# Kernel optimization log

Measured on AMD Instinct MI355X. Metric: run time of the kernel, lower is better.

Reference implementation:

```python
import jax, jax.numpy as jnp
import numpy as np

B, S, HID = 2, 1024, 2048
NH, NKV, HD = 16, 4, 128
SCALE = 1.0 / np.sqrt(HD)
ROPE_BASE = 10000.0
EPS = 1e-6


def setup_inputs() -> dict:
    key = jax.random.key(0)
    ks = jax.random.split(key, 5)
    std = 0.02
    return {
        "hidden_states": jax.random.normal(ks[0], (B, S, HID), jnp.float32),
        "Wq": jax.random.normal(ks[1], (NH * HD, HID), jnp.float32) * std,
        "Wk": jax.random.normal(ks[2], (NKV * HD, HID), jnp.float32) * std,
        "Wv": jax.random.normal(ks[3], (NKV * HD, HID), jnp.float32) * std,
        "Wo": jax.random.normal(ks[4], (HID, HID), jnp.float32) * std,
        "q_norm_w": jnp.ones((HD,), jnp.float32),
        "k_norm_w": jnp.ones((HD,), jnp.float32),
    }


def _rope(x):
    # x: [B, H, S, D]; half-split rotary
    d2 = HD // 2
    inv_freq = 1.0 / (ROPE_BASE ** (jnp.arange(0, HD, 2, dtype=jnp.float32) / HD))
    ang = jnp.arange(S, dtype=jnp.float32)[:, None] * inv_freq[None, :]  # [S, d2]
    cos, sin = jnp.cos(ang), jnp.sin(ang)
    x1, x2 = x[..., :d2], x[..., d2:]
    return jnp.concatenate([x1 * cos - x2 * sin, x1 * sin + x2 * cos], axis=-1)


def _rms(x, w):
    var = jnp.mean(jnp.square(x), axis=-1, keepdims=True)
    return x * jax.lax.rsqrt(var + EPS) * w


def reference(hidden_states, Wq, Wk, Wv, Wo, q_norm_w, k_norm_w):
    b, s, _ = hidden_states.shape
    # projections (no bias)
    q = (hidden_states @ Wq.T).reshape(b, s, NH, HD).transpose(0, 2, 1, 3)
    k = (hidden_states @ Wk.T).reshape(b, s, NKV, HD).transpose(0, 2, 1, 3)
    v = (hidden_states @ Wv.T).reshape(b, s, NKV, HD).transpose(0, 2, 1, 3)
    # RoPE then per-head-dim RMS qk-norm (shared params across heads)
    q, k = _rope(q), _rope(k)
    q, k = _rms(q, q_norm_w), _rms(k, k_norm_w)
    # GQA: repeat kv heads
    groups = NH // NKV
    k = jnp.repeat(k, groups, axis=1)
    v = jnp.repeat(v, groups, axis=1)
    # stick-breaking attention, strictly causal (attend_current=False), no normalize
    logits = jnp.einsum("bhid,bhjd->bhij", q, k) * SCALE  # [B,H,S,S]
    log_p = jax.nn.log_sigmoid(logits)
    log_om = jax.nn.log_sigmoid(-logits)  # log(1 - p)
    i = jnp.arange(s)
    mask = i[None, :] < i[:, None]  # j < i
    masked_om = jnp.where(mask, log_om, 0.0)
    # cum[i,j] = sum_{j < k < i} log(1-p[i,k]) : exclusive reversed cumsum
    cum = jnp.flip(jnp.cumsum(jnp.flip(masked_om, -1), -1), -1) - masked_om
    att = jnp.where(mask, jnp.exp(log_p + cum), 0.0)
    o = jnp.einsum("bhij,bhjd->bhid", att, v)
    o = o.transpose(0, 2, 1, 3).reshape(b, s, NH * HD)
    return o @ Wo.T
```

## Files before the change

kernel.cpp:

```cpp
#include <hip/hip_runtime.h>
#include <math.h>

#define B_    2
#define S_    1024
#define HID_  2048
#define NH_   16
#define NKV_  4
#define HD_   128
#define GROUPS (NH_ / NKV_)
#define SCALE_ 0.08838834764831845f

#define NZ_   2
#define QPSZ  4194304
#define KPSZ  1048576

typedef _Float16 f16x8 __attribute__((ext_vector_type(8)));
typedef _Float16 f16x4 __attribute__((ext_vector_type(4)));
typedef float    f32x4 __attribute__((ext_vector_type(4)));

__device__ __forceinline__ void async_copy16(const void* g, void* l) {
    __builtin_amdgcn_global_load_lds(
        (const __attribute__((address_space(1))) void*)g,
        (__attribute__((address_space(3))) void*)l, 16, 0, 0);
}

__device__ __forceinline__ int dpp_swap1(int x) {
    return __builtin_amdgcn_update_dpp(0, x, 0xB1, 0xF, 0xF, true);
}

__global__ __launch_bounds__(256) void cast5_f16(
    const float4* __restrict__ s0, ushort4* __restrict__ d0, int n0,
    const float4* __restrict__ s1, ushort4* __restrict__ d1, int n1,
    const float4* __restrict__ s2, ushort4* __restrict__ d2, int n2,
    const float4* __restrict__ s3, ushort4* __restrict__ d3, int n3,
    const float4* __restrict__ s4, ushort4* __restrict__ d4, int n4)
{
    int i = blockIdx.x * 256 + threadIdx.x;
    const float4* s; ushort4* d; int idx;
    if (i < n0)                          { s = s0; d = d0; idx = i; }
    else if (i < n0 + n1)                { s = s1; d = d1; idx = i - n0; }
    else if (i < n0 + n1 + n2)           { s = s2; d = d2; idx = i - n0 - n1; }
    else if (i < n0 + n1 + n2 + n3)      { s = s3; d = d3; idx = i - n0 - n1 - n2; }
    else if (i < n0 + n1 + n2 + n3 + n4) { s = s4; d = d4; idx = i - n0 - n1 - n2 - n3; }
    else return;
    float4 v = s[idx];
    _Float16 a = (_Float16)v.x, b = (_Float16)v.y,
             c = (_Float16)v.z, e = (_Float16)v.w;
    ushort4 o;
    o.x = *(unsigned short*)&a; o.y = *(unsigned short*)&b;
    o.z = *(unsigned short*)&c; o.w = *(unsigned short*)&e;
    d[idx] = o;
}

__global__ __launch_bounds__(256) void qkv_gemm(
    const _Float16* __restrict__ A,
    const _Float16* __restrict__ Wq,
    const _Float16* __restrict__ Wk,
    const _Float16* __restrict__ Wv,
    _Float16* __restrict__ Qp,
    _Float16* __restrict__ Kp,
    _Float16* __restrict__ Vp)
{
    __shared__ __align__(16) unsigned char smem[32768];

    const int tid  = threadIdx.x;
    const int lane = tid & 63, wave = tid >> 6;
    const int wr = (wave >> 1) * 64, wc = (wave & 1) * 64;
    const int bm = blockIdx.y * 128;
    const int bt = blockIdx.x;
    const int z  = blockIdx.z;
    const int kbase = z * (HID_ / NZ_);

    const _Float16* Wsel;
    _Float16* Csel;
    int nrow0, heads;
    if (bt < 16)      { Wsel = Wq; Csel = Qp + (size_t)z * QPSZ; nrow0 = bt * 128;        heads = NH_;  }
    else if (bt < 20) { Wsel = Wk; Csel = Kp + (size_t)z * KPSZ; nrow0 = (bt - 16) * 128; heads = NKV_; }
    else              { Wsel = Wv; Csel = Vp + (size_t)z * KPSZ; nrow0 = (bt - 20) * 128; heads = NKV_; }

    const int srow = 32 * wave + (lane >> 2);
    const int scol = (((lane & 3) ^ ((lane >> 3) & 3))) * 8;
    const _Float16* Ag = A    + (size_t)(bm + srow)    * HID_ + kbase + scol;
    const _Float16* Wg = Wsel + (size_t)(nrow0 + srow) * HID_ + kbase + scol;

    const unsigned aoff = (unsigned)(wave * 2048);

    f32x4 acc[4][4];
    const f32x4 fz = {0.f, 0.f, 0.f, 0.f};
#pragma unroll
    for (int i = 0; i < 4; i++)
#pragma unroll
        for (int j = 0; j < 4; j++) acc[i][j] = fz;

    const int ml = lane & 15, kg = lane >> 4;
    const int kgx = kg ^ ((ml >> 1) & 3);

#define QKV_STAGE(d, k0) do {                                                 \
        _Float16* la_ = (_Float16*)(smem + (d) * 16384 + aoff);               \
        _Float16* lw_ = (_Float16*)(smem + (d) * 16384 + 8192 + aoff);        \
        async_copy16(Ag + (k0), la_);                                         \
        async_copy16(Ag + (k0) + (size_t)16 * HID_, la_ + 16 * 32);           \
        async_copy16(Wg + (k0), lw_);                                         \
        async_copy16(Wg + (k0) + (size_t)16 * HID_, lw_ + 16 * 32);           \
    } while (0)

#define QKV_COMPUTE(d) do {                                                   \
        const _Float16* tA = (const _Float16*)(smem + (d) * 16384);           \
        const _Float16* tW = (const _Float16*)(smem + (d) * 16384 + 8192);    \
        f16x8 a[4], b[4];                                                     \
        _Pragma("unroll")                                                     \
        for (int mi = 0; mi < 4; mi++)                                        \
            a[mi] = *(const f16x8*)&tA[(wr + mi * 16 + ml) * 32 + kgx * 8];   \
        _Pragma("unroll")                                                     \
        for (int ni = 0; ni < 4; ni++)                                        \
            b[ni] = *(const f16x8*)&tW[(wc + ni * 16 + ml) * 32 + kgx * 8];   \
        _Pragma("unroll")                                                     \
        for (int mi = 0; mi < 4; mi++)                                        \
            _Pragma("unroll")                                                 \
            for (int ni = 0; ni < 4; ni++)                                    \
                acc[mi][ni] = __builtin_amdgcn_mfma_f32_16x16x32_f16(         \
                    a[mi], b[ni], acc[mi][ni], 0, 0, 0);                      \
    } while (0)

    QKV_STAGE(0, 0);
    asm volatile("s_waitcnt vmcnt(0)" ::: "memory");
    __builtin_amdgcn_s_barrier();

    int d = 0;
    for (int t = 0; t < 31; t++) {
        QKV_STAGE(d ^ 1, (t + 1) * 32);
        asm volatile("s_waitcnt vmcnt(4)" ::: "memory");
        __builtin_amdgcn_s_barrier();
        __builtin_amdgcn_sched_barrier(0);

        QKV_COMPUTE(d);

        __builtin_amdgcn_sched_barrier(0);
        __builtin_amdgcn_s_barrier();
        d ^= 1;
    }
    asm volatile("s_waitcnt vmcnt(0)" ::: "memory");
    __builtin_amdgcn_s_barrier();
    __builtin_amdgcn_sched_barrier(0);
    QKV_COMPUTE(d);
#undef QKV_STAGE
#undef QKV_COMPUTE

#pragma unroll
    for (int mi = 0; mi < 4; mi++) {
#pragma unroll
        for (int ni = 0; ni < 4; ni++) {
#pragma unroll
            for (int r = 0; r < 4; r++) {
                int m = bm + wr + mi * 16 + kg * 4 + r;
                int n = nrow0 + wc + ni * 16 + ml;
                int hh = n >> 7, d2 = n & 127;
                int b_ = m >> 10, s = m & 1023;
                size_t idx = (((size_t)(b_ * heads + hh)) * S_ + s) * HD_ + d2;
                Csel[idx] = (_Float16)acc[mi][ni][r];
            }
        }
    }
}

__global__ __launch_bounds__(512) void out_gemm(
    const _Float16* __restrict__ A,
    const _Float16* __restrict__ W,
    float* __restrict__ Cout)
{
    __shared__ __align__(16) unsigned char smem[66560];

    const int tid  = threadIdx.x;
    const int lane = tid & 63, wave = tid >> 6;
    const int kh = wave >> 2;
    const int wv = wave & 3;
    const int wr = (wv >> 1) * 64, wc = (wv & 1) * 64;
    const int bm = blockIdx.y * 128, bn = blockIdx.x * 128;
    const int kbase = kh * (HID_ / 2);

    const int srow = 32 * wv + (lane >> 2);
    const int scol = (((lane & 3) ^ ((lane >> 3) & 3))) * 8;
    const _Float16* Ag = A + (size_t)(bm + srow) * HID_ + kbase + scol;
    const _Float16* Wg = W + (size_t)(bn + srow) * HID_ + kbase + scol;

    const unsigned aoff = (unsigned)(kh * 8192 + 32 * wv * 64);
    const unsigned woff = (unsigned)(16384 + kh * 8192 + 32 * wv * 64);

    f32x4 acc[4][4];
    const f32x4 fz = {0.f, 0.f, 0.f, 0.f};
#pragma unroll
    for (int i = 0; i < 4; i++)
#pragma unroll
        for (int j = 0; j < 4; j++) acc[i][j] = fz;

    const int ml = lane & 15, kg = lane >> 4;
    const int kgx = kg ^ ((ml >> 1) & 3);

#define OG_STAGE(d, k0) do {                                                  \
        _Float16* la_ = (_Float16*)(smem + (d) * 32768 + aoff);               \
        _Float16* lw_ = (_Float16*)(smem + (d) * 32768 + woff);               \
        async_copy16(Ag + (k0), la_);                                         \
        async_copy16(Ag + (k0) + (size_t)16 * HID_, la_ + 16 * 32);           \
        async_copy16(Wg + (k0), lw_);                                         \
        async_copy16(Wg + (k0) + (size_t)16 * HID_, lw_ + 16 * 32);           \
    } while (0)

#define OG_COMPUTE(d) do {                                                    \
        const _Float16* tA = (const _Float16*)(smem + (d) * 32768 + kh * 8192);\
        const _Float16* tW = (const _Float16*)(smem + (d) * 32768 + 16384 + kh * 8192);\
        f16x8 a[4], b[4];                                                     \
        _Pragma("unroll")                                                     \
        for (int mi = 0; mi < 4; mi++)                                        \
            a[mi] = *(const f16x8*)&tA[(wr + mi * 16 + ml) * 32 + kgx * 8];   \
        _Pragma("unroll")                                                     \
        for (int ni = 0; ni < 4; ni++)                                        \
            b[ni] = *(const f16x8*)&tW[(wc + ni * 16 + ml) * 32 + kgx * 8];   \
        _Pragma("unroll")                                                     \
        for (int mi = 0; mi < 4; mi++)                                        \
            _Pragma("unroll")                                                 \
            for (int ni = 0; ni < 4; ni++)                                    \
                acc[mi][ni] = __builtin_amdgcn_mfma_f32_16x16x32_f16(         \
                    a[mi], b[ni], acc[mi][ni], 0, 0, 0);                      \
    } while (0)

    OG_STAGE(0, 0);
    asm volatile("s_waitcnt vmcnt(0)" ::: "memory");
    __builtin_amdgcn_s_barrier();

    int d = 0;
    for (int t = 0; t < 31; t++) {
        OG_STAGE(d ^ 1, (t + 1) * 32);
        asm volatile("s_waitcnt vmcnt(4)" ::: "memory");
        __builtin_amdgcn_s_barrier();
        __builtin_amdgcn_sched_barrier(0);

        OG_COMPUTE(d);

        __builtin_amdgcn_sched_barrier(0);
        __builtin_amdgcn_s_barrier();
        d ^= 1;
    }
    asm volatile("s_waitcnt vmcnt(0)" ::: "memory");
    __builtin_amdgcn_s_barrier();
    __builtin_amdgcn_sched_barrier(0);
    OG_COMPUTE(d);
#undef OG_STAGE
#undef OG_COMPUTE

    __syncthreads();
    float* red = (float*)smem;
    float* rp  = red + ((size_t)(wv * 64 + lane)) * 65;
    if (kh == 1) {
#pragma unroll
        for (int mi = 0; mi < 4; mi++)
#pragma unroll
            for (int ni = 0; ni < 4; ni++)
#pragma unroll
                for (int r = 0; r < 4; r++)
                    rp[mi * 16 + ni * 4 + r] = acc[mi][ni][r];
    }
    __syncthreads();
    if (kh == 0) {
#pragma unroll
        for (int mi = 0; mi < 4; mi++)
#pragma unroll
            for (int ni = 0; ni < 4; ni++)
#pragma unroll
                for (int r = 0; r < 4; r++) {
                    float v = acc[mi][ni][r] + rp[mi * 16 + ni * 4 + r];
                    int m = bm + wr + mi * 16 + kg * 4 + r;
                    int n = bn + wc + ni * 16 + ml;
                    Cout[(size_t)m * HID_ + n] = v;
                }
    }
}

__global__ __launch_bounds__(256) void rope_rms_v(
    const _Float16* __restrict__ Qp, const _Float16* __restrict__ Kp,
    const _Float16* __restrict__ Vp,
    const float* __restrict__ qw, const float* __restrict__ kw,
    _Float16* __restrict__ Qout, _Float16* __restrict__ Kout,
    _Float16* __restrict__ Vout)
{
    int row = blockIdx.x * 4 + (threadIdx.x >> 6);
    int lane = threadIdx.x & 63;

    if (row >= 40960) {
        int lrow = row - 40960;
        size_t off = (size_t)lrow * HD_ + lane * 2;
        float a0 = 0.f, a1 = 0.f;
#pragma unroll
        for (int zp = 0; zp < NZ_; zp++) {
            a0 += (float)Vp[(size_t)zp * KPSZ + off];
            a1 += (float)Vp[(size_t)zp * KPSZ + off + 1];
        }
        _Float16* q = Vout + (size_t)lrow * HD_;
        q[lane * 2]     = (_Float16)a0;
        q[lane * 2 + 1] = (_Float16)a1;
        return;
    }

    bool isQ = row < 32768;
    int lrow = isQ ? row : row - 32768;
    const _Float16* p0 = isQ ? Qp : Kp;
    size_t psz = isQ ? QPSZ : KPSZ;
    _Float16* q = (isQ ? Qout : Kout) + (size_t)lrow * HD_;
    const float* w = isQ ? qw : kw;
    int s = row & (S_ - 1);

    size_t base = (size_t)lrow * HD_;
    float x1 = 0.f, x2 = 0.f;
#pragma unroll
    for (int zp = 0; zp < NZ_; zp++) {
        x1 += (float)p0[(size_t)zp * psz + base + lane];
        x2 += (float)p0[(size_t)zp * psz + base + lane + 64];
    }

    float invf = __builtin_amdgcn_exp2f(-(float)lane * 0.2076205059304601f);
    float ang = (float)s * invf;
    float sn = __sinf(ang);
    float c  = __cosf(ang);

    float y1 = x1 * c - x2 * sn;
    float y2 = x1 * sn + x2 * c;

    float ss = y1 * y1 + y2 * y2;
#pragma unroll
    for (int off = 32; off > 0; off >>= 1) ss += __shfl_xor(ss, off);

    float scl = rsqrtf(ss * (1.0f / 128.0f) + 1e-6f);
    q[lane]      = (_Float16)(y1 * scl * w[lane]);
    q[lane + 64] = (_Float16)(y2 * scl * w[lane + 64]);
}

#define QK_STR 136
#define VT_STR 72
#define SS_STR 68
#define AT_STR 72

__global__ __launch_bounds__(512) void stick_attn(
    const _Float16* __restrict__ Q, const _Float16* __restrict__ K,
    const _Float16* __restrict__ V, _Float16* __restrict__ AO)
{
    __shared__ __align__(16) _Float16 Qs[64][QK_STR];
    __shared__ __align__(16) _Float16 Ks[64][QK_STR];
    __shared__ __align__(16) _Float16 Vt[128][VT_STR];
    __shared__ __align__(16) float    Ss[64][SS_STR];
    __shared__ __align__(16) _Float16 atts[64][AT_STR];
    __shared__ float paccs[64];

    const int bid = blockIdx.x;
    const int slot = bid & 255, phase = bid >> 8;
    const int hb = slot >> 3, iw = slot & 7;
    const int b = hb >> 4, h = hb & 15;
    const int qb = phase ? iw : 15 - iw;

    const int kvh = h / GROUPS;
    const int tid = threadIdx.x;
    const int lane = tid & 63, wave = tid >> 6;
    const int qw = wave >> 1;
    const int kh = wave & 1;
    const int ml = lane & 15, quad = lane >> 4;

    const _Float16* Kbase = K + ((size_t)(b * NKV_ + kvh) * S_) * HD_;
    const _Float16* Vbase = V + ((size_t)(b * NKV_ + kvh) * S_) * HD_;

    const f32x4 fz = {0.f, 0.f, 0.f, 0.f};

    const int qi0 = qb * 64;
    const _Float16* Qbase = Q + ((size_t)(b * NH_ + h) * S_ + qi0) * HD_;

    const int kr = tid >> 4, kc = (tid & 15) * 8;
    const _Float16* Vrow = Vbase + (size_t)lane * HD_ + wave * 16;

    f16x8 kA, kB, vA, vB;
    {
        const _Float16* kp = Kbase + (size_t)(qb * 64 + kr) * HD_ + kc;
        kA = *(const f16x8*)(kp);
        kB = *(const f16x8*)(kp + (size_t)32 * HD_);
        const _Float16* vp = Vrow + (size_t)(qb * 64) * HD_;
        vA = *(const f16x8*)(vp);
        vB = *(const f16x8*)(vp + 8);
    }

    for (int idx = tid; idx < 64 * 16; idx += 512) {
        int r = idx >> 4, c8 = (idx & 15) * 8;
        *(f16x8*)&Qs[r][c8] = *(const f16x8*)(Qbase + r * HD_ + c8);
    }
    if (tid < 64) paccs[tid] = 1.f;
    __syncthreads();

    f16x8 aq[4];
#pragma unroll
    for (int ks = 0; ks < 4; ks++)
        aq[ks] = *(const f16x8*)&Qs[qw * 16 + ml][ks * 32 + quad * 8];

    f32x4 accO[4] = {fz, fz, fz, fz};

    for (int kb = qb; kb >= 0; --kb) {
        __syncthreads();

        *(f16x8*)&Ks[kr][kc]      = kA;
        *(f16x8*)&Ks[kr + 32][kc] = kB;

        {
            int4 i0 = *(int4*)&vA, i1 = *(int4*)&vB;
            int4 p0, p1;
            p0.x = dpp_swap1(i0.x); p0.y = dpp_swap1(i0.y);
            p0.z = dpp_swap1(i0.z); p0.w = dpp_swap1(i0.w);
            p1.x = dpp_swap1(i1.x); p1.y = dpp_swap1(i1.y);
            p1.z = dpp_swap1(i1.z); p1.w = dpp_swap1(i1.w);
            bool ev = !(lane & 1);
            int4 al = ev ? i0 : p1;
            int4 bh = ev ? p0 : i1;
            int r0w = wave * 16 + (ev ? 0 : 8);
            int colk = lane & ~1;
            int ac[4] = {al.x, al.y, al.z, al.w};
            int bc[4] = {bh.x, bh.y, bh.z, bh.w};
#pragma unroll
            for (int i = 0; i < 8; i++) {
                int c = i >> 1;
                unsigned pack = (i & 1)
                    ? (((unsigned)ac[c] >> 16) | ((unsigned)bc[c] & 0xffff0000u))
                    : (((unsigned)ac[c] & 0xffffu) | ((unsigned)bc[c] << 16));
                *(unsigned*)&Vt[r0w + i][colk] = pack;
            }
        }
        __syncthreads();

        if (kb > 0) {
            const _Float16* kp = Kbase + (size_t)((kb - 1) * 64 + kr) * HD_ + kc;
            kA = *(const f16x8*)(kp);
            kB = *(const f16x8*)(kp + (size_t)32 * HD_);
            const _Float16* vp = Vrow + (size_t)((kb - 1) * 64) * HD_;
            vA = *(const f16x8*)(vp);
            vB = *(const f16x8*)(vp + 8);
        }

        f32x4 accS[2] = {fz, fz};
        __builtin_amdgcn_s_setprio(1);
#pragma unroll
        for (int ks = 0; ks < 4; ks++) {
#pragma unroll
            for (int ni = 0; ni < 2; ni++) {
                f16x8 bf = *(const f16x8*)
                    &Ks[kh * 32 + ni * 16 + ml][ks * 32 + quad * 8];
                accS[ni] = __builtin_amdgcn_mfma_f32_16x16x32_f16(
                    aq[ks], bf, accS[ni], 0, 0, 0);
            }
        }
        __builtin_amdgcn_s_setprio(0);
#pragma unroll
        for (int ni = 0; ni < 2; ni++)
#pragma unroll
            for (int r = 0; r < 4; r++)
                Ss[qw * 16 + quad * 4 + r][kh * 32 + ni * 16 + ml] =
                    accS[ni][r] * SCALE_;
        __syncthreads();

        {
            int q = tid >> 3, seg = tid & 7;
            int qg = qi0 + q;
            int j0 = kb * 64 + seg * 8;
            float4 s0 = *(float4*)&Ss[q][seg * 8];
            float4 s1 = *(float4*)&Ss[q][seg * 8 + 4];
            float L[8] = {s0.x, s0.y, s0.z, s0.w, s1.x, s1.y, s1.z, s1.w};
            float sv[8], om[8];
#pragma unroll
            for (int i = 0; i < 8; i++) {
                float u = __expf(L[i]);
                float o = __builtin_amdgcn_rcpf(1.f + u);
                bool valid = (j0 + i < qg);
                om[i] = valid ? o : 1.f;
                sv[i] = valid ? (1.f - o) : 0.f;
            }
            float suf = 1.f, lo[8];
#pragma unroll
            for (int i = 7; i >= 0; --i) {
                lo[i] = suf; suf *= om[i];
            }
            float x = suf;
#pragma unroll
            for (int off = 1; off < 8; off <<= 1) {
                float y = __shfl_down(x, off);
                if (seg + off < 8) x *= y;
            }
            float bx = __shfl_down(x, 1);
            float base = (seg == 7) ? 1.f : bx;
            float paccq = paccs[q];
            float pb = base * paccq;
            f16x8 av;
#pragma unroll
            for (int i = 0; i < 8; i++)
                av[i] = (_Float16)(sv[i] * lo[i] * pb);
            *(f16x8*)&atts[q][seg * 8] = av;
            if (seg == 0) paccs[q] = paccq * x;
        }
        __syncthreads();

        __builtin_amdgcn_s_setprio(1);
#pragma unroll
        for (int ks = 0; ks < 2; ks++) {
            f16x8 ap = *(const f16x8*)&atts[qw * 16 + ml][ks * 32 + quad * 8];
#pragma unroll
            for (int ni = 0; ni < 4; ni++) {
                f16x8 bv = *(const f16x8*)
                    &Vt[kh * 64 + ni * 16 + ml][ks * 32 + quad * 8];
                accO[ni] = __builtin_amdgcn_mfma_f32_16x16x32_f16(
                    ap, bv, accO[ni], 0, 0, 0);
            }
        }
        __builtin_amdgcn_s_setprio(0);
    }

#pragma unroll
    for (int ni = 0; ni < 4; ni++) {
#pragma unroll
        for (int r = 0; r < 4; r++) {
            int qg = qi0 + qw * 16 + quad * 4 + r;
            int d = kh * 64 + ni * 16 + ml;
            AO[((size_t)(b * S_ + qg) * NH_ + h) * HD_ + d] =
                (_Float16)accO[ni][r];
        }
    }
}

extern "C" void kernel_launch(void* const* d_in, const int* in_sizes, int n_in,
                              void* d_out, int out_size, void* d_ws, size_t ws_size,
                              hipStream_t stream)
{
    const float* hs = (const float*)d_in[0];
    const float* Wq = (const float*)d_in[1];
    const float* Wk = (const float*)d_in[2];
    const float* Wv = (const float*)d_in[3];
    const float* Wo = (const float*)d_in[4];
    const float* qw = (const float*)d_in[5];
    const float* kw = (const float*)d_in[6];
    float* out = (float*)d_out;

    _Float16* Qp  = (_Float16*)d_ws;
    _Float16* Kp  = Qp + (size_t)NZ_ * QPSZ;
    _Float16* Vp  = Kp + (size_t)NZ_ * KPSZ;
    _Float16* hsh = Vp + (size_t)NZ_ * KPSZ;
    _Float16* Wqh = hsh + 4194304;
    _Float16* Wkh = Wqh + 4194304;
    _Float16* Wvh = Wkh + 1048576;
    _Float16* Woh = Wvh + 1048576;
    _Float16* Qh  = Woh + 4194304;
    _Float16* Kh  = Qh + 4194304;
    _Float16* Vh  = Kh + 1048576;
    _Float16* AOh = hsh;

    dim3 blk(256);

    cast5_f16<<<14336, blk, 0, stream>>>(
        (const float4*)hs, (ushort4*)hsh, 1048576,
        (const float4*)Wq, (ushort4*)Wqh, 1048576,
        (const float4*)Wk, (ushort4*)Wkh, 262144,
        (const float4*)Wv, (ushort4*)Wvh, 262144,
        (const float4*)Wo, (ushort4*)Woh, 1048576);

    qkv_gemm<<<dim3(24, 16, NZ_), blk, 0, stream>>>(hsh, Wqh, Wkh, Wvh,
                                                    Qp, Kp, Vp);

    rope_rms_v<<<dim3(49152 / 4), blk, 0, stream>>>(
        Qp, Kp, Vp, qw, kw, Qh, Kh, Vh);

    stick_attn<<<dim3(512), dim3(512), 0, stream>>>(Qh, Kh, Vh, AOh);

    out_gemm<<<dim3(16, 16), dim3(512), 0, stream>>>(AOh, Woh, out);
}
```

Measured before the change: 209.2 us.

## Replace split-K global partials in QKV GEMM with in-block split-K LDS reduction

The QKV projection used to split K across two grid slices, each writing fp16 partial results to global memory, and the RoPE/RMS kernel then summed the two partials. Now each 512-thread block splits K across two wave groups over a 128x64 tile and reduces the partials through shared memory before one store. The RoPE and V-copy paths read a single buffer. This removes the extra partial-buffer traffic and the summation work, at the cost of narrower N tiles (more A reloads), higher LDS use and an in-block reduction step.

```diff
diff --git a/kernel.cpp b/kernel.cpp
--- a/kernel.cpp
+++ b/kernel.cpp
@@ -9,10 +9,6 @@
 #define HD_   128
 #define GROUPS (NH_ / NKV_)
 #define SCALE_ 0.08838834764831845f
-
-#define NZ_   2
-#define QPSZ  4194304
-#define KPSZ  1048576
 
 typedef _Float16 f16x8 __attribute__((ext_vector_type(8)));
 typedef _Float16 f16x4 __attribute__((ext_vector_type(4)));
@@ -52,7 +48,7 @@
     d[idx] = o;
 }
 
-__global__ __launch_bounds__(256) void qkv_gemm(
+__global__ __launch_bounds__(512) void qkv_gemm(
     const _Float16* __restrict__ A,
     const _Float16* __restrict__ Wq,
     const _Float16* __restrict__ Wk,
@@ -61,63 +57,65 @@
     _Float16* __restrict__ Kp,
     _Float16* __restrict__ Vp)
 {
-    __shared__ __align__(16) unsigned char smem[32768];
+    __shared__ __align__(16) unsigned char smem[49152];
 
     const int tid  = threadIdx.x;
     const int lane = tid & 63, wave = tid >> 6;
-    const int wr = (wave >> 1) * 64, wc = (wave & 1) * 64;
+    const int kh = wave >> 2;
+    const int wv = wave & 3;
+    const int wr = (wv >> 1) * 64, wc = (wv & 1) * 32;
     const int bm = blockIdx.y * 128;
     const int bt = blockIdx.x;
-    const int z  = blockIdx.z;
-    const int kbase = z * (HID_ / NZ_);
+    const int kbase = kh * (HID_ / 2);
 
     const _Float16* Wsel;
     _Float16* Csel;
     int nrow0, heads;
-    if (bt < 16)      { Wsel = Wq; Csel = Qp + (size_t)z * QPSZ; nrow0 = bt * 128;        heads = NH_;  }
-    else if (bt < 20) { Wsel = Wk; Csel = Kp + (size_t)z * KPSZ; nrow0 = (bt - 16) * 128; heads = NKV_; }
-    else              { Wsel = Wv; Csel = Vp + (size_t)z * KPSZ; nrow0 = (bt - 20) * 128; heads = NKV_; }
-
-    const int srow = 32 * wave + (lane >> 2);
-    const int scol = (((lane & 3) ^ ((lane >> 3) & 3))) * 8;
+    if (bt < 32)      { Wsel = Wq; Csel = Qp; nrow0 = bt * 64;        heads = NH_;  }
+    else if (bt < 40) { Wsel = Wk; Csel = Kp; nrow0 = (bt - 32) * 64; heads = NKV_; }
+    else              { Wsel = Wv; Csel = Vp; nrow0 = (bt - 40) * 64; heads = NKV_; }
+
+    const int srow = 32 * wv + (lane >> 2);
+    const int wrow = 16 * wv + (lane >> 2);
+    const int scol = ((lane & 3) ^ ((lane >> 3) & 3)) * 8;
     const _Float16* Ag = A    + (size_t)(bm + srow)    * HID_ + kbase + scol;
-    const _Float16* Wg = Wsel + (size_t)(nrow0 + srow) * HID_ + kbase + scol;
-
-    const unsigned aoff = (unsigned)(wave * 2048);
-
-    f32x4 acc[4][4];
+    const _Float16* Wg = Wsel + (size_t)(nrow0 + wrow) * HID_ + kbase + scol;
+
+    const unsigned aoff = (unsigned)(kh * 8192 + wv * 2048);
+    const unsigned woff = (unsigned)(16384 + kh * 4096 + wv * 1024);
+
+    f32x4 acc[4][2];
     const f32x4 fz = {0.f, 0.f, 0.f, 0.f};
 #pragma unroll
     for (int i = 0; i < 4; i++)
 #pragma unroll
-        for (int j = 0; j < 4; j++) acc[i][j] = fz;
+        for (int j = 0; j < 2; j++) acc[i][j] = fz;
 
     const int ml = lane & 15, kg = lane >> 4;
     const int kgx = kg ^ ((ml >> 1) & 3);
 
 #define QKV_STAGE(d, k0) do {                                                 \
-        _Float16* la_ = (_Float16*)(smem + (d) * 16384 + aoff);               \
-        _Float16* lw_ = (_Float16*)(smem + (d) * 16384 + 8192 + aoff);        \
+        _Float16* la_ = (_Float16*)(smem + (d) * 24576 + aoff);               \
+        _Float16* lw_ = (_Float16*)(smem + (d) * 24576 + woff);               \
         async_copy16(Ag + (k0), la_);                                         \
         async_copy16(Ag + (k0) + (size_t)16 * HID_, la_ + 16 * 32);           \
         async_copy16(Wg + (k0), lw_);                                         \
-        async_copy16(Wg + (k0) + (size_t)16 * HID_, lw_ + 16 * 32);           \
     } while (0)
 
 #define QKV_COMPUTE(d) do {                                                   \
-        const _Float16* tA = (const _Float16*)(smem + (d) * 16384);           \
-        const _Float16* tW = (const _Float16*)(smem + (d) * 16384 + 8192);    \
-        f16x8 a[4], b[4];                                                     \
+        const _Float16* tA = (const _Float16*)(smem + (d) * 24576 + kh * 8192);\
+        const _Float16* tW = (const _Float16*)(smem + (d) * 24576 + 16384 + kh * 4096);\
+        f16x8 a[4], b[2];                                                     \
         _Pragma("unroll")                                                     \
         for (int mi = 0; mi < 4; mi++)                                        \
             a[mi] = *(const f16x8*)&tA[(wr + mi * 16 + ml) * 32 + kgx * 8];   \
         _Pragma("unroll")                                                     \
-        for (int ni = 0; ni < 4; ni++)                                        \
+        for (int ni = 0; ni < 2; ni++)                                        \
             b[ni] = *(const f16x8*)&tW[(wc + ni * 16 + ml) * 32 + kgx * 8];   \
         _Pragma("unroll")                                                     \
         for (int mi = 0; mi < 4; mi++)                                        \
             _Pragma("unroll")                                                 \
-            for (int ni = 0; ni < 4; ni++)                                    \
+            for (int ni = 0; ni < 2; ni++)                                    \
                 acc[mi][ni] = __builtin_amdgcn_mfma_f32_16x16x32_f16(         \
                     a[mi], b[ni], acc[mi][ni], 0, 0, 0);                      \
     } while (0)
@@ -129,7 +127,7 @@
     int d = 0;
     for (int t = 0; t < 31; t++) {
         QKV_STAGE(d ^ 1, (t + 1) * 32);
-        asm volatile("s_waitcnt vmcnt(4)" ::: "memory");
+        asm volatile("s_waitcnt vmcnt(3)" ::: "memory");
         __builtin_amdgcn_s_barrier();
         __builtin_amdgcn_sched_barrier(0);
 
@@ -146,20 +144,34 @@
 #undef QKV_STAGE
 #undef QKV_COMPUTE
 
-#pragma unroll
-    for (int mi = 0; mi < 4; mi++) {
-#pragma unroll
-        for (int ni = 0; ni < 4; ni++) {
-#pragma unroll
-            for (int r = 0; r < 4; r++) {
-                int m = bm + wr + mi * 16 + kg * 4 + r;
-                int n = nrow0 + wc + ni * 16 + ml;
-                int hh = n >> 7, d2 = n & 127;
-                int b_ = m >> 10, s = m & 1023;
-                size_t idx = (((size_t)(b_ * heads + hh)) * S_ + s) * HD_ + d2;
-                Csel[idx] = (_Float16)acc[mi][ni][r];
-            }
-        }
+    __syncthreads();
+    float* red = (float*)smem;
+    float* rp  = red + ((size_t)(wv * 64 + lane)) * 33;
+    if (kh == 1) {
+#pragma unroll
+        for (int mi = 0; mi < 4; mi++)
+#pragma unroll
+            for (int ni = 0; ni < 2; ni++)
+#pragma unroll
+                for (int r = 0; r < 4; r++)
+                    rp[mi * 8 + ni * 4 + r] = acc[mi][ni][r];
+    }
+    __syncthreads();
+    if (kh == 0) {
+#pragma unroll
+        for (int mi = 0; mi < 4; mi++)
+#pragma unroll
+            for (int ni = 0; ni < 2; ni++)
+#pragma unroll
+                for (int r = 0; r < 4; r++) {
+                    float v = acc[mi][ni][r] + rp[mi * 8 + ni * 4 + r];
+                    int m = bm + wr + mi * 16 + kg * 4 + r;
+                    int n = nrow0 + wc + ni * 16 + ml;
+                    int hh = n >> 7, d2 = n & 127;
+                    int b_ = m >> 10, s = m & 1023;
+                    size_t idx = (((size_t)(b_ * heads + hh)) * S_ + s) * HD_ + d2;
+                    Csel[idx] = (_Float16)v;
+                }
     }
 }
 
@@ -288,33 +300,20 @@
     if (row >= 40960) {
         int lrow = row - 40960;
         size_t off = (size_t)lrow * HD_ + lane * 2;
-        float a0 = 0.f, a1 = 0.f;
-#pragma unroll
-        for (int zp = 0; zp < NZ_; zp++) {
-            a0 += (float)Vp[(size_t)zp * KPSZ + off];
-            a1 += (float)Vp[(size_t)zp * KPSZ + off + 1];
-        }
-        _Float16* q = Vout + (size_t)lrow * HD_;
-        q[lane * 2]     = (_Float16)a0;
-        q[lane * 2 + 1] = (_Float16)a1;
+        *(ushort2*)(Vout + off) = *(const ushort2*)(Vp + off);
         return;
     }
 
     bool isQ = row < 32768;
     int lrow = isQ ? row : row - 32768;
     const _Float16* p0 = isQ ? Qp : Kp;
-    size_t psz = isQ ? QPSZ : KPSZ;
     _Float16* q = (isQ ? Qout : Kout) + (size_t)lrow * HD_;
     const float* w = isQ ? qw : kw;
     int s = row & (S_ - 1);
 
     size_t base = (size_t)lrow * HD_;
-    float x1 = 0.f, x2 = 0.f;
-#pragma unroll
-    for (int zp = 0; zp < NZ_; zp++) {
-        x1 += (float)p0[(size_t)zp * psz + base + lane];
-        x2 += (float)p0[(size_t)zp * psz + base + lane + 64];
-    }
+    float x1 = (float)p0[base + lane];
+    float x2 = (float)p0[base + lane + 64];
 
     float invf = __builtin_amdgcn_exp2f(-(float)lane * 0.2076205059304601f);
     float ang = (float)s * invf;
@@ -539,9 +538,9 @@
     float* out = (float*)d_out;
 
     _Float16* Qp  = (_Float16*)d_ws;
-    _Float16* Kp  = Qp + (size_t)NZ_ * QPSZ;
-    _Float16* Vp  = Kp + (size_t)NZ_ * KPSZ;
-    _Float16* hsh = Vp + (size_t)NZ_ * KPSZ;
+    _Float16* Kp  = Qp + 4194304;
+    _Float16* Vp  = Kp + 1048576;
+    _Float16* hsh = Vp + 1048576;
     _Float16* Wqh = hsh + 4194304;
     _Float16* Wkh = Wqh + 4194304;
     _Float16* Wvh = Wkh + 1048576;
@@ -560,8 +559,8 @@
         (const float4*)Wv, (ushort4*)Wvh, 262144,
         (const float4*)Wo, (ushort4*)Woh, 1048576);
 
-    qkv_gemm<<<dim3(24, 16, NZ_), blk, 0, stream>>>(hsh, Wqh, Wkh, Wvh,
-                                                    Qp, Kp, Vp);
+    qkv_gemm<<<dim3(48, 16), dim3(512), 0, stream>>>(hsh, Wqh, Wkh, Wvh,
+                                                     Qp, Kp, Vp);
 
     rope_rms_v<<<dim3(49152 / 4), blk, 0, stream>>>(
         Qp, Kp, Vp, qw, kw, Qh, Kh, Vh);
```

After: 213.7 us. 1.02x slower.

## Triple-buffer LDS tiles in QKV and output GEMMs to drop trailing barrier

Applied to the files above, without the earlier changes.

Both GEMM kernels go from a double-buffered to a triple-buffered LDS ring and drop the second per-iteration barrier, along with the prologue wait. The goal is to halve synchronization per k-step and let the next tile's load overlap more fully with MFMA compute. In exchange, LDS use grows (48KB and 96KB per block), which may cut occupancy. With only one barrier per step, correctness depends on the three-buffer distance keeping writes away from the tile still being read.

```diff
diff --git a/kernel.cpp b/kernel.cpp
--- a/kernel.cpp
+++ b/kernel.cpp
@@ -61,7 +61,7 @@
     _Float16* __restrict__ Kp,
     _Float16* __restrict__ Vp)
 {
-    __shared__ __align__(16) unsigned char smem[32768];
+    __shared__ __align__(16) unsigned char smem[49152];
 
     const int tid  = threadIdx.x;
     const int lane = tid & 63, wave = tid >> 6;
@@ -123,26 +123,21 @@
     } while (0)
 
     QKV_STAGE(0, 0);
-    asm volatile("s_waitcnt vmcnt(0)" ::: "memory");
-    __builtin_amdgcn_s_barrier();
-
-    int d = 0;
+    int cbuf = 0;
     for (int t = 0; t < 31; t++) {
-        QKV_STAGE(d ^ 1, (t + 1) * 32);
+        int nbuf = (cbuf == 2) ? 0 : cbuf + 1;
+        QKV_STAGE(nbuf, (t + 1) * 32);
         asm volatile("s_waitcnt vmcnt(4)" ::: "memory");
         __builtin_amdgcn_s_barrier();
         __builtin_amdgcn_sched_barrier(0);
 
-        QKV_COMPUTE(d);
-
-        __builtin_amdgcn_sched_barrier(0);
-        __builtin_amdgcn_s_barrier();
-        d ^= 1;
+        QKV_COMPUTE(cbuf);
+        cbuf = nbuf;
     }
     asm volatile("s_waitcnt vmcnt(0)" ::: "memory");
     __builtin_amdgcn_s_barrier();
     __builtin_amdgcn_sched_barrier(0);
-    QKV_COMPUTE(d);
+    QKV_COMPUTE(cbuf);
 #undef QKV_STAGE
 #undef QKV_COMPUTE
 
@@ -168,7 +163,7 @@
     const _Float16* __restrict__ W,
     float* __restrict__ Cout)
 {
-    __shared__ __align__(16) unsigned char smem[66560];
+    __shared__ __align__(16) unsigned char smem[98304];
 
     const int tid  = threadIdx.x;
     const int lane = tid & 63, wave = tid >> 6;
@@ -224,26 +219,21 @@
     } while (0)
 
     OG_STAGE(0, 0);
-    asm volatile("s_waitcnt vmcnt(0)" ::: "memory");
-    __builtin_amdgcn_s_barrier();
-
-    int d = 0;
+    int cbuf = 0;
     for (int t = 0; t < 31; t++) {
-        OG_STAGE(d ^ 1, (t + 1) * 32);
+        int nbuf = (cbuf == 2) ? 0 : cbuf + 1;
+        OG_STAGE(nbuf, (t + 1) * 32);
         asm volatile("s_waitcnt vmcnt(4)" ::: "memory");
         __builtin_amdgcn_s_barrier();
         __builtin_amdgcn_sched_barrier(0);
 
-        OG_COMPUTE(d);
-
-        __builtin_amdgcn_sched_barrier(0);
-        __builtin_amdgcn_s_barrier();
-        d ^= 1;
+        OG_COMPUTE(cbuf);
+        cbuf = nbuf;
     }
     asm volatile("s_waitcnt vmcnt(0)" ::: "memory");
     __builtin_amdgcn_s_barrier();
     __builtin_amdgcn_sched_barrier(0);
-    OG_COMPUTE(d);
+    OG_COMPUTE(cbuf);
 #undef OG_STAGE
 #undef OG_COMPUTE
 
```

New measurement: 207.9 us. No clear change (-0.6%).
